# Performance work log

Hardware: AMD Instinct MI355X
Metric: run time of the kernel (lower is better)

Reference implementation:

```python
import jax, jax.numpy as jnp
import numpy as np

B, H, W, C, UNITS = 16, 64, 64, 64, 128

def setup_inputs() -> dict:
    key = jax.random.key(0)
    k1, k2 = jax.random.split(key)
    x = jax.random.normal(k1, (B, H, W, C), dtype=jnp.float32)
    # 'random_normal' keras initializer defaults to stddev=0.05
    w = jax.random.normal(k2, (UNITS, C, W, H), dtype=jnp.float32) * 0.05
    return {"x": x, "w": w}

def reference(x, w):
    # Original: transpose NHWC->NCHW, broadcasted matmul (W,H)@(H,W),
    # reduce-sum over C, transpose back, relu.
    # Fused contraction: y[b,i,j,u] = sum_{c,h} w[u,c,i,h] * x[b,h,j,c]
    y = jnp.einsum('ucih,bhjc->biju', w, x)  # (B, W, W, units)
    return jax.nn.relu(y)
```

## Files before the change

### kernel.cpp

```cpp
#include <hip/hip_runtime.h>
#include <hip/hip_bf16.h>


typedef __attribute__((ext_vector_type(4))) float f32x4;
typedef __attribute__((ext_vector_type(8))) short bf16x8;
typedef __attribute__((ext_vector_type(4))) unsigned int u32x4;
typedef __attribute__((ext_vector_type(2))) unsigned int u32x2;
typedef unsigned short ushort_t;

static __device__ __forceinline__ unsigned int cvt_pk_bf16(float lo, float hi) {
  unsigned int r;
  asm("v_cvt_pk_bf16_f32 %0, %1, %2" : "=v"(r) : "v"(lo), "v"(hi));
  return r;
}

static __device__ __forceinline__ void async_copy16(void* lds, const void* g) {
  __builtin_amdgcn_global_load_lds(
      (const __attribute__((address_space(1))) unsigned int*)g,
      (__attribute__((address_space(3))) unsigned int*)lds, 16, 0, 0);
}

__global__ __launch_bounds__(256)
void conv_x(const float* __restrict__ X, ushort_t* __restrict__ Xb, int n4) {
  int idx = blockIdx.x * 256 + threadIdx.x;
  const int stride = gridDim.x * 256;
  for (; idx < n4; idx += stride) {
    f32x4 v = ((const f32x4*)X)[idx];
    u32x2 o;
    o.x = cvt_pk_bf16(v.x, v.y);
    o.y = cvt_pk_bf16(v.z, v.w);
    ((u32x2*)Xb)[idx] = o;
  }
}

__global__ __launch_bounds__(256)
void conv_w(const float* __restrict__ W, ushort_t* __restrict__ Wb) {
  __shared__ float T[64][65];
  const int bid = blockIdx.x;
  const int u = bid >> 6;
  const int i = bid & 63;
  const int t = threadIdx.x;

  const int hq = t & 15;
  const int c4 = t >> 4;
  const float* base = W + (((size_t)u * 64) * 64 + i) * 64;
#pragma unroll
  for (int it = 0; it < 4; ++it) {
    const int c = it * 16 + c4;
    f32x4 v = *(const f32x4*)(base + (size_t)c * 4096 + hq * 4);
    *(f32x4*)&T[c][hq * 4] = v;
  }
  __syncthreads();

  const int h = t >> 2;
  const int c0 = (t & 3) * 16;
  unsigned int pk[8];
#pragma unroll
  for (int q = 0; q < 8; ++q)
    pk[q] = cvt_pk_bf16(T[c0 + 2 * q][h], T[c0 + 2 * q + 1][h]);
  ushort_t* out = Wb + (((size_t)i * 128 + u) * 64 + h) * 64 + c0;
  ((u32x4*)out)[0] = *(u32x4*)&pk[0];
  ((u32x4*)out)[1] = *(u32x4*)&pk[4];
}

__global__ __launch_bounds__(512, 2)
void gemm8(const ushort_t* __restrict__ Xb, const ushort_t* __restrict__ Wb,
           float* __restrict__ O) {
  __shared__ ushort_t As[3][128 * 64];
  __shared__ ushort_t Bs[3][256 * 64];

  const int tid = threadIdx.x;
  const int lane = tid & 63;
  const int wid = tid >> 6;
  const int wm = wid >> 2;
  const int wn = wid & 3;

  const int bid = blockIdx.x;
  const int wg = (bid & 7) * 32 + (bid >> 3);
  const int mt = wg & 7;
  const int nt2 = wg >> 3;

  const char* XbB = (const char*)Xb;
  const char* WbB = (const char*)Wb;

  int a_dst[2]; size_t a_src[2];
#pragma unroll
  for (int it = 0; it < 2; ++it) {
    const int flat = it * 8192 + tid * 16;
    const int row = flat >> 7;
    const int p = (flat >> 4) & 7;
    const int b = mt * 2 + (row >> 6);
    const int j = row & 63;
    a_dst[it] = flat;
    a_src[it] = (size_t)b * 524288 + (size_t)j * 128 + ((p ^ (row & 7)) << 4);
  }
  int b_dst[4]; size_t b_src[4];
#pragma unroll
  for (int it = 0; it < 4; ++it) {
    const int flat = it * 8192 + tid * 16;
    const int nl = flat >> 7;
    const int p = (flat >> 4) & 7;
    b_dst[it] = flat;
    b_src[it] = (size_t)(nt2 * 256 + nl) * 8192 + ((p ^ (nl & 7)) << 4);
  }

  int a_ro[2][4], b_ro[2][4];
#pragma unroll
  for (int kk = 0; kk < 2; ++kk) {
#pragma unroll
    for (int f = 0; f < 4; ++f) {
      int row = wm * 64 + f * 16 + (lane & 15);
      int byte0 = row * 128 + kk * 64 + (lane >> 4) * 16;
      a_ro[kk][f] = byte0 ^ ((row & 7) << 4);
      row = wn * 64 + f * 16 + (lane & 15);
      byte0 = row * 128 + kk * 64 + (lane >> 4) * 16;
      b_ro[kk][f] = byte0 ^ ((row & 7) << 4);
    }
  }

  f32x4 acc[4][4];
#pragma unroll
  for (int i = 0; i < 4; ++i)
#pragma unroll
    for (int j = 0; j < 4; ++j) acc[i][j] = (f32x4){0.f, 0.f, 0.f, 0.f};

  auto stageA = [&](int buf, int h) {
    char* la = (char*)&As[buf][0];
#pragma unroll
    for (int it = 0; it < 2; ++it)
      async_copy16(la + a_dst[it], XbB + a_src[it] + (size_t)h * 8192);
  };
  auto stageB0 = [&](int buf, int h) {
    char* lb = (char*)&Bs[buf][0];
    async_copy16(lb + b_dst[0], WbB + b_src[0] + (size_t)h * 128);
  };
  auto stageB123 = [&](int buf, int h) {
    char* lb = (char*)&Bs[buf][0];
#pragma unroll
    for (int it = 1; it < 4; ++it)
      async_copy16(lb + b_dst[it], WbB + b_src[it] + (size_t)h * 128);
  };

  stageA(0, 0); stageB0(0, 0); stageB123(0, 0);
  stageA(1, 1); stageB0(1, 1); stageB123(1, 1);
  asm volatile("s_waitcnt vmcnt(6)" ::: "memory");
  __builtin_amdgcn_s_barrier();

  int cur = 0, pre = 2;
  for (int t = 0; t < 64; ++t) {
    const int h2 = t + 2;
    const char* ab = (const char*)&As[cur][0];
    const char* bb = (const char*)&Bs[cur][0];
    bf16x8 af[4], bfr[4];

    __builtin_amdgcn_sched_barrier(0);
#pragma unroll
    for (int f = 0; f < 4; ++f) af[f] = *(const bf16x8*)(ab + a_ro[0][f]);
#pragma unroll
    for (int f = 0; f < 4; ++f) bfr[f] = *(const bf16x8*)(bb + b_ro[0][f]);
    if (h2 < 64) { stageA(pre, h2); stageB0(pre, h2); }
    __builtin_amdgcn_s_barrier();
    __builtin_amdgcn_s_setprio(1);
#pragma unroll
    for (int mf = 0; mf < 4; ++mf)
#pragma unroll
      for (int nf = 0; nf < 4; ++nf)
        acc[mf][nf] = __builtin_amdgcn_mfma_f32_16x16x32_bf16(
            af[mf], bfr[nf], acc[mf][nf], 0, 0, 0);
    __builtin_amdgcn_s_setprio(0);
    __builtin_amdgcn_s_barrier();

    __builtin_amdgcn_sched_barrier(0);
#pragma unroll
    for (int f = 0; f < 4; ++f) af[f] = *(const bf16x8*)(ab + a_ro[1][f]);
#pragma unroll
    for (int f = 0; f < 4; ++f) bfr[f] = *(const bf16x8*)(bb + b_ro[1][f]);
    if (h2 < 64) stageB123(pre, h2);
    __builtin_amdgcn_s_barrier();
    __builtin_amdgcn_s_setprio(1);
#pragma unroll
    for (int mf = 0; mf < 4; ++mf)
#pragma unroll
      for (int nf = 0; nf < 4; ++nf)
        acc[mf][nf] = __builtin_amdgcn_mfma_f32_16x16x32_bf16(
            af[mf], bfr[nf], acc[mf][nf], 0, 0, 0);
    __builtin_amdgcn_s_setprio(0);
    if (t < 62) {
      asm volatile("s_waitcnt vmcnt(6)" ::: "memory");
    } else {
      asm volatile("s_waitcnt vmcnt(0)" ::: "memory");
    }
    __builtin_amdgcn_s_barrier();

    cur = (cur == 2) ? 0 : cur + 1;
    pre = (pre == 2) ? 0 : pre + 1;
  }

  const int rbase = (lane >> 4) * 4;
  const int cn = lane & 15;
#pragma unroll
  for (int mf = 0; mf < 4; ++mf) {
#pragma unroll
    for (int r = 0; r < 4; ++r) {
      const int ml = wm * 64 + mf * 16 + rbase + r;
      const int m = mt * 128 + ml;
      const int b = m >> 6;
      const int j = m & 63;
#pragma unroll
      for (int nf = 0; nf < 4; ++nf) {
        const int nloc = wn * 64 + nf * 16 + cn;
        const int i = nt2 * 2 + (nloc >> 7);
        const int u = nloc & 127;
        O[(((size_t)b * 64 + i) * 64 + j) * 128 + u] = fmaxf(acc[mf][nf][r], 0.f);
      }
    }
  }
}

__global__ __launch_bounds__(256, 2)
void fused_gemm(const float* __restrict__ X, const float* __restrict__ Wt,
                float* __restrict__ O) {
  __shared__ ushort_t As[2][128 * 64];
  __shared__ ushort_t Bs[2][128 * 64];
  const int tid = threadIdx.x;
  const int lane = tid & 63;
  const int wid = tid >> 6;
  const int wm = wid >> 1;
  const int wn = wid & 1;
  const int bid = blockIdx.x;
  const int wg = (bid & 7) * 64 + (bid >> 3);
  const int mt = wg & 7;
  const int nt = wg >> 3;
  const int a_ml = tid >> 1;
  const int a_hp = (tid & 1) * 2;
  const int a_b = (mt * 128 + a_ml) >> 6;
  const int a_j = a_ml & 63;
  const float* a_base = X + ((size_t)a_b << 18) + ((size_t)a_j << 6);
  const int b_nl = tid >> 1;
  const int b_c8 = (tid & 1) * 8;
  const float* b_base = Wt + ((size_t)b_nl << 18) + ((size_t)nt << 6);
  f32x4 ra[2][4];
  f32x4 rb[8];
  f32x4 acc[4][4];
#pragma unroll
  for (int i = 0; i < 4; ++i)
#pragma unroll
    for (int j = 0; j < 4; ++j) acc[i][j] = (f32x4){0.f, 0.f, 0.f, 0.f};
  auto stage_load = [&](int t) {
    const int th = t & 15;
    const int tc = t >> 4;
    const int c0 = tc * 16;
    const int h0 = th * 4;
#pragma unroll
    for (int s = 0; s < 2; ++s) {
      const float* p = a_base + (size_t)(h0 + a_hp + s) * 4096 + c0;
#pragma unroll
      for (int q = 0; q < 4; ++q) ra[s][q] = ((const f32x4*)p)[q];
    }
#pragma unroll
    for (int q = 0; q < 8; ++q)
      rb[q] = *(const f32x4*)(b_base + (size_t)(c0 + b_c8 + q) * 4096 + h0);
  };
  auto stage_write = [&](int buf) {
    char* abase = (char*)&As[buf][0];
    const int swa = (a_ml & 7) << 4;
#pragma unroll
    for (int s = 0; s < 2; ++s) {
      u32x4 lo, hi;
      lo.x = cvt_pk_bf16(ra[s][0].x, ra[s][0].y);
      lo.y = cvt_pk_bf16(ra[s][0].z, ra[s][0].w);
      lo.z = cvt_pk_bf16(ra[s][1].x, ra[s][1].y);
      lo.w = cvt_pk_bf16(ra[s][1].z, ra[s][1].w);
      hi.x = cvt_pk_bf16(ra[s][2].x, ra[s][2].y);
      hi.y = cvt_pk_bf16(ra[s][2].z, ra[s][2].w);
      hi.z = cvt_pk_bf16(ra[s][3].x, ra[s][3].y);
      hi.w = cvt_pk_bf16(ra[s][3].z, ra[s][3].w);
      const int byte0 = a_ml * 128 + (a_hp + s) * 32;
      *(u32x4*)(abase + (byte0 ^ swa)) = lo;
      *(u32x4*)(abase + ((byte0 + 16) ^ swa)) = hi;
    }
    char* bbase = (char*)&Bs[buf][0];
    const int swb = (b_nl & 7) << 4;
#pragma unroll
    for (int hl = 0; hl < 4; ++hl) {
      u32x4 v;
      v.x = cvt_pk_bf16(rb[0][hl], rb[1][hl]);
      v.y = cvt_pk_bf16(rb[2][hl], rb[3][hl]);
      v.z = cvt_pk_bf16(rb[4][hl], rb[5][hl]);
      v.w = cvt_pk_bf16(rb[6][hl], rb[7][hl]);
      const int byte0 = b_nl * 128 + (hl * 16 + b_c8) * 2;
      *(u32x4*)(bbase + (byte0 ^ swb)) = v;
    }
  };
  auto compute = [&](int buf) {
    const char* abase = (const char*)&As[buf][0];
    const char* bbase = (const char*)&Bs[buf][0];
#pragma unroll
    for (int kk = 0; kk < 2; ++kk) {
      bf16x8 af[4], bfr[4];
#pragma unroll
      for (int mf = 0; mf < 4; ++mf) {
        const int row = wm * 64 + mf * 16 + (lane & 15);
        const int byte0 = row * 128 + kk * 64 + (lane >> 4) * 16;
        af[mf] = *(const bf16x8*)(abase + (byte0 ^ ((row & 7) << 4)));
      }
#pragma unroll
      for (int nf = 0; nf < 4; ++nf) {
        const int row = wn * 64 + nf * 16 + (lane & 15);
        const int byte0 = row * 128 + kk * 64 + (lane >> 4) * 16;
        bfr[nf] = *(const bf16x8*)(bbase + (byte0 ^ ((row & 7) << 4)));
      }
#pragma unroll
      for (int mf = 0; mf < 4; ++mf)
#pragma unroll
        for (int nf = 0; nf < 4; ++nf)
          acc[mf][nf] = __builtin_amdgcn_mfma_f32_16x16x32_bf16(
              af[mf], bfr[nf], acc[mf][nf], 0, 0, 0);
    }
  };
  stage_load(0);
  stage_write(0);
  __syncthreads();
  int cur = 0;
  for (int t = 0; t < 64; ++t) {
    if (t + 1 < 64) stage_load(t + 1);
    compute(cur);
    if (t + 1 < 64) stage_write(cur ^ 1);
    __syncthreads();
    cur ^= 1;
  }
  const int rbase = (lane >> 4) * 4;
  const int cn = lane & 15;
#pragma unroll
  for (int mf = 0; mf < 4; ++mf) {
#pragma unroll
    for (int r = 0; r < 4; ++r) {
      const int ml = wm * 64 + mf * 16 + rbase + r;
      const int m = mt * 128 + ml;
      const int b = m >> 6;
      const int j = m & 63;
      float* orow = O + (((size_t)b * 64 + nt) * 64 + j) * 128;
#pragma unroll
      for (int nf = 0; nf < 4; ++nf) {
        const int u = wn * 64 + nf * 16 + cn;
        orow[u] = fmaxf(acc[mf][nf][r], 0.f);
      }
    }
  }
}

extern "C" void kernel_launch(void* const* d_in, const int* in_sizes, int n_in,
                              void* d_out, int out_size, void* d_ws, size_t ws_size,
                              hipStream_t stream) {
  const float* x = (const float*)d_in[0];
  const float* w = (const float*)d_in[1];
  float* out = (float*)d_out;

  const size_t XB_BYTES = (size_t)16 * 64 * 64 * 64 * 2;
  const size_t WB_BYTES = (size_t)64 * 128 * 64 * 64 * 2;

  if (ws_size >= XB_BYTES + WB_BYTES) {
    ushort_t* Xb = (ushort_t*)d_ws;
    ushort_t* Wb = (ushort_t*)((char*)d_ws + XB_BYTES);
    hipLaunchKernelGGL(conv_x, dim3(1024), dim3(256), 0, stream, x, Xb,
                       (int)(16 * 64 * 64 * 64 / 4));
    hipLaunchKernelGGL(conv_w, dim3(8192), dim3(256), 0, stream, w, Wb);
    hipLaunchKernelGGL(gemm8, dim3(256), dim3(512), 0, stream, Xb, Wb, out);
  } else {
    hipLaunchKernelGGL(fused_gemm, dim3(512), dim3(256), 0, stream, x, w, out);
  }
}
```

Measured before the change: 109.6 us.

## Collapse ping-pong barrier schedule into single-phase stage, load, compute loop

Replaces the two-half main loop, which interleaved LDS fragment reads, split async copies, inner barriers and setprio toggles, with one phase per k-step. That phase issues all async global-to-LDS copies for the prefetch buffer, reads both k-halves of fragments, then runs all 32 MFMAs. This removes two barriers per iteration and the priority switching, and lets the compiler schedule LDS reads against MFMAs freely. The cost is more live fragment registers and no explicit interleaving of memory issue with math.

```diff
diff --git a/kernel.cpp b/kernel.cpp
--- a/kernel.cpp
+++ b/kernel.cpp
@@ -124,25 +124,19 @@
 #pragma unroll
     for (int j = 0; j < 4; ++j) acc[i][j] = (f32x4){0.f, 0.f, 0.f, 0.f};
 
-  auto stageA = [&](int buf, int h) {
+  auto stage = [&](int buf, int h) {
     char* la = (char*)&As[buf][0];
+    char* lb = (char*)&Bs[buf][0];
 #pragma unroll
     for (int it = 0; it < 2; ++it)
       async_copy16(la + a_dst[it], XbB + a_src[it] + (size_t)h * 8192);
-  };
-  auto stageB0 = [&](int buf, int h) {
-    char* lb = (char*)&Bs[buf][0];
-    async_copy16(lb + b_dst[0], WbB + b_src[0] + (size_t)h * 128);
-  };
-  auto stageB123 = [&](int buf, int h) {
-    char* lb = (char*)&Bs[buf][0];
-#pragma unroll
-    for (int it = 1; it < 4; ++it)
+#pragma unroll
+    for (int it = 0; it < 4; ++it)
       async_copy16(lb + b_dst[it], WbB + b_src[it] + (size_t)h * 128);
   };
 
-  stageA(0, 0); stageB0(0, 0); stageB123(0, 0);
-  stageA(1, 1); stageB0(1, 1); stageB123(1, 1);
+  stage(0, 0);
+  stage(1, 1);
   asm volatile("s_waitcnt vmcnt(6)" ::: "memory");
   __builtin_amdgcn_s_barrier();
 
@@ -151,40 +145,27 @@
     const int h2 = t + 2;
     const char* ab = (const char*)&As[cur][0];
     const char* bb = (const char*)&Bs[cur][0];
-    bf16x8 af[4], bfr[4];
-
-    __builtin_amdgcn_sched_barrier(0);
-#pragma unroll
-    for (int f = 0; f < 4; ++f) af[f] = *(const bf16x8*)(ab + a_ro[0][f]);
-#pragma unroll
-    for (int f = 0; f < 4; ++f) bfr[f] = *(const bf16x8*)(bb + b_ro[0][f]);
-    if (h2 < 64) { stageA(pre, h2); stageB0(pre, h2); }
-    __builtin_amdgcn_s_barrier();
-    __builtin_amdgcn_s_setprio(1);
-#pragma unroll
-    for (int mf = 0; mf < 4; ++mf)
-#pragma unroll
-      for (int nf = 0; nf < 4; ++nf)
-        acc[mf][nf] = __builtin_amdgcn_mfma_f32_16x16x32_bf16(
-            af[mf], bfr[nf], acc[mf][nf], 0, 0, 0);
-    __builtin_amdgcn_s_setprio(0);
-    __builtin_amdgcn_s_barrier();
-
-    __builtin_amdgcn_sched_barrier(0);
-#pragma unroll
-    for (int f = 0; f < 4; ++f) af[f] = *(const bf16x8*)(ab + a_ro[1][f]);
-#pragma unroll
-    for (int f = 0; f < 4; ++f) bfr[f] = *(const bf16x8*)(bb + b_ro[1][f]);
-    if (h2 < 64) stageB123(pre, h2);
-    __builtin_amdgcn_s_barrier();
-    __builtin_amdgcn_s_setprio(1);
-#pragma unroll
-    for (int mf = 0; mf < 4; ++mf)
-#pragma unroll
-      for (int nf = 0; nf < 4; ++nf)
-        acc[mf][nf] = __builtin_amdgcn_mfma_f32_16x16x32_bf16(
-            af[mf], bfr[nf], acc[mf][nf], 0, 0, 0);
-    __builtin_amdgcn_s_setprio(0);
+
+    if (h2 < 64) stage(pre, h2);
+
+    bf16x8 af[2][4], bfr[2][4];
+#pragma unroll
+    for (int kk = 0; kk < 2; ++kk) {
+#pragma unroll
+      for (int f = 0; f < 4; ++f) af[kk][f] = *(const bf16x8*)(ab + a_ro[kk][f]);
+#pragma unroll
+      for (int f = 0; f < 4; ++f) bfr[kk][f] = *(const bf16x8*)(bb + b_ro[kk][f]);
+    }
+#pragma unroll
+    for (int kk = 0; kk < 2; ++kk)
+#pragma unroll
+      for (int mf = 0; mf < 4; ++mf)
+#pragma unroll
+        for (int nf = 0; nf < 4; ++nf)
+          acc[mf][nf] = __builtin_amdgcn_mfma_f32_16x16x32_bf16(
+              af[kk][mf], bfr[kk][nf], acc[mf][nf], 0, 0, 0);
+
+    asm volatile("s_waitcnt lgkmcnt(0)" ::: "memory");
     if (t < 62) {
       asm volatile("s_waitcnt vmcnt(6)" ::: "memory");
     } else {
```

Measured after the change: 125.0 us. 14.1% more time.

## Double-buffer LDS fragment reads in registers to overlap with MFMA

Applied to the files above, without the earlier changes.

Restructures the main GEMM loop so each half-step's LDS fragment loads are issued one phase ahead into a second register set. The MFMAs then consume fragments loaded in the previous phase. The global-to-LDS wait moves earlier in the iteration, with a tighter vmcnt count, so the next buffer is ready before its first fragments are read. This hides LDS read latency behind matrix math, at the cost of more VGPRs and a tighter ordering of async-copy waits.

```diff
diff --git a/kernel.cpp b/kernel.cpp
--- a/kernel.cpp
+++ b/kernel.cpp
@@ -124,41 +124,59 @@
 #pragma unroll
     for (int j = 0; j < 4; ++j) acc[i][j] = (f32x4){0.f, 0.f, 0.f, 0.f};
 
-  auto stageA = [&](int buf, int h) {
+  auto stage = [&](int buf, int h) {
     char* la = (char*)&As[buf][0];
+    char* lb = (char*)&Bs[buf][0];
 #pragma unroll
     for (int it = 0; it < 2; ++it)
       async_copy16(la + a_dst[it], XbB + a_src[it] + (size_t)h * 8192);
-  };
-  auto stageB0 = [&](int buf, int h) {
+#pragma unroll
+    for (int it = 0; it < 4; ++it)
+      async_copy16(lb + b_dst[it], WbB + b_src[it] + (size_t)h * 128);
+  };
+  auto stage3a = [&](int buf, int h) {
+    char* la = (char*)&As[buf][0];
     char* lb = (char*)&Bs[buf][0];
+#pragma unroll
+    for (int it = 0; it < 2; ++it)
+      async_copy16(la + a_dst[it], XbB + a_src[it] + (size_t)h * 8192);
     async_copy16(lb + b_dst[0], WbB + b_src[0] + (size_t)h * 128);
   };
-  auto stageB123 = [&](int buf, int h) {
+  auto stage3b = [&](int buf, int h) {
     char* lb = (char*)&Bs[buf][0];
 #pragma unroll
     for (int it = 1; it < 4; ++it)
       async_copy16(lb + b_dst[it], WbB + b_src[it] + (size_t)h * 128);
   };
 
-  stageA(0, 0); stageB0(0, 0); stageB123(0, 0);
-  stageA(1, 1); stageB0(1, 1); stageB123(1, 1);
+  bf16x8 fa0[4], fb0[4], fa1[4], fb1[4];
+
+  auto readFrags = [&](bf16x8 (&fa)[4], bf16x8 (&fb)[4], int buf, int kk) {
+    const char* ab = (const char*)&As[buf][0];
+    const char* bb = (const char*)&Bs[buf][0];
+#pragma unroll
+    for (int f = 0; f < 4; ++f) fa[f] = *(const bf16x8*)(ab + a_ro[kk][f]);
+#pragma unroll
+    for (int f = 0; f < 4; ++f) fb[f] = *(const bf16x8*)(bb + b_ro[kk][f]);
+  };
+
+  stage(0, 0);
+  stage(1, 1);
   asm volatile("s_waitcnt vmcnt(6)" ::: "memory");
   __builtin_amdgcn_s_barrier();
-
-  int cur = 0, pre = 2;
+  readFrags(fa0, fb0, 0, 0);
+
+  int cur = 0, nxt = 1, pre = 2;
   for (int t = 0; t < 64; ++t) {
-    const int h2 = t + 2;
-    const char* ab = (const char*)&As[cur][0];
-    const char* bb = (const char*)&Bs[cur][0];
-    bf16x8 af[4], bfr[4];
-
     __builtin_amdgcn_sched_barrier(0);
-#pragma unroll
-    for (int f = 0; f < 4; ++f) af[f] = *(const bf16x8*)(ab + a_ro[0][f]);
-#pragma unroll
-    for (int f = 0; f < 4; ++f) bfr[f] = *(const bf16x8*)(bb + b_ro[0][f]);
-    if (h2 < 64) { stageA(pre, h2); stageB0(pre, h2); }
+    readFrags(fa1, fb1, cur, 1);
+    if (t + 2 < 64) stage3a(pre, t + 2);
+    if (t < 62) {
+      asm volatile("s_waitcnt vmcnt(3)" ::: "memory");
+    } else {
+      asm volatile("s_waitcnt vmcnt(0)" ::: "memory");
+    }
+    __builtin_amdgcn_sched_barrier(0);
     __builtin_amdgcn_s_barrier();
     __builtin_amdgcn_s_setprio(1);
 #pragma unroll
@@ -166,16 +184,14 @@
 #pragma unroll
       for (int nf = 0; nf < 4; ++nf)
         acc[mf][nf] = __builtin_amdgcn_mfma_f32_16x16x32_bf16(
-            af[mf], bfr[nf], acc[mf][nf], 0, 0, 0);
+            fa0[mf], fb0[nf], acc[mf][nf], 0, 0, 0);
     __builtin_amdgcn_s_setprio(0);
     __builtin_amdgcn_s_barrier();
 
     __builtin_amdgcn_sched_barrier(0);
-#pragma unroll
-    for (int f = 0; f < 4; ++f) af[f] = *(const bf16x8*)(ab + a_ro[1][f]);
-#pragma unroll
-    for (int f = 0; f < 4; ++f) bfr[f] = *(const bf16x8*)(bb + b_ro[1][f]);
-    if (h2 < 64) stageB123(pre, h2);
+    if (t + 1 < 64) readFrags(fa0, fb0, nxt, 0);
+    if (t + 2 < 64) stage3b(pre, t + 2);
+    __builtin_amdgcn_sched_barrier(0);
     __builtin_amdgcn_s_barrier();
     __builtin_amdgcn_s_setprio(1);
 #pragma unroll
@@ -183,16 +199,12 @@
 #pragma unroll
       for (int nf = 0; nf < 4; ++nf)
         acc[mf][nf] = __builtin_amdgcn_mfma_f32_16x16x32_bf16(
-            af[mf], bfr[nf], acc[mf][nf], 0, 0, 0);
+            fa1[mf], fb1[nf], acc[mf][nf], 0, 0, 0);
     __builtin_amdgcn_s_setprio(0);
-    if (t < 62) {
-      asm volatile("s_waitcnt vmcnt(6)" ::: "memory");
-    } else {
-      asm volatile("s_waitcnt vmcnt(0)" ::: "memory");
-    }
     __builtin_amdgcn_s_barrier();
 
     cur = (cur == 2) ? 0 : cur + 1;
+    nxt = (nxt == 2) ? 0 : nxt + 1;
     pre = (pre == 2) ? 0 : pre + 1;
   }
 
```

After: 107.1 us, median of 2. 1.02x faster.
